# Performance work log

Measured on AMD Instinct MI355X. Metric: run time of the kernel, lower is better.

Reference implementation:

```python
import jax, jax.numpy as jnp
import numpy as np

B, S, I, H, O, L = 256, 512, 256, 256, 256, 64


def setup_inputs() -> dict:
    key = jax.random.key(0)
    ks = jax.random.split(key, 12)
    def lin(k, fan_in, fan_out):
        kw, kb = jax.random.split(k)
        lim = 1.0 / np.sqrt(fan_in)
        W = jax.random.uniform(kw, (fan_in, fan_out), jnp.float32, -lim, lim)
        b = jax.random.uniform(kb, (fan_out,), jnp.float32, -lim, lim)
        return W, b
    x = jax.random.normal(ks[0], (B, S, I), jnp.float32)
    W1x, b1x = lin(ks[1], I, H)   # rnn1.Wax
    W1a, b1a = lin(ks[2], H, H)   # rnn1.Waa
    W2x, b2x = lin(ks[3], O, H)   # rnn2.Wax
    W2a, b2a = lin(ks[4], H, H)   # rnn2.Waa
    Wy, by = lin(ks[5], H, O)     # Wya
    return {"x": x, "W1x": W1x, "b1x": b1x, "W1a": W1a, "b1a": b1a,
            "W2x": W2x, "b2x": b2x, "W2a": W2a, "b2a": b2a, "Wy": Wy, "by": by}


def reference(x, W1x, b1x, W1a, b1a, W2x, b2x, W2a, b2a, Wy, by):
    batch = x.shape[0]
    a0 = jnp.zeros((batch, W1a.shape[0]), x.dtype)  # a[:, -1] is zeros at encoder start

    # Encoder: a_t = tanh(Wax(x_t) + Waa(a_{t-1}))
    def enc_step(a, x_t):
        a = jnp.tanh(x_t @ W1x + b1x + a @ W1a + b1a)
        return a, None
    a_last, _ = jax.lax.scan(enc_step, a0, jnp.swapaxes(x, 0, 1))  # [S,B,I] scan

    # Torch code: y_pred[:,0] set from encoder, then decoder reads y_pred[:,i]
    # BEFORE overwriting it -> input is y0 at i=0, zeros for i>0.
    y0 = jax.nn.sigmoid(a_last @ Wy + by)  # [B,O]
    zero_in = jnp.zeros_like(y0)

    def dec_step(a, i):
        inp = jnp.where(i == 0, y0, zero_in)
        a = jnp.tanh(inp @ W2x + b2x + a @ W2a + b2a)
        y = jax.nn.sigmoid(a @ Wy + by)
        return a, y
    _, ys = jax.lax.scan(dec_step, a_last, jnp.arange(L))  # ys: [L,B,O]
    return jnp.swapaxes(ys, 0, 1)  # [B,L,O]
```

## Files before the change

kernel.cpp:

```cpp
#include <hip/hip_runtime.h>

typedef unsigned short u16;
typedef unsigned int   u32;
typedef __attribute__((ext_vector_type(8))) __bf16 bf16x8;
typedef __attribute__((ext_vector_type(8))) u16    u16x8;
typedef __attribute__((ext_vector_type(4))) float  f32x4;
typedef __attribute__((ext_vector_type(4))) u32    u32x4;
typedef __attribute__((ext_vector_type(2))) u32    u32x2;

#define MFMA16(a,b,c) __builtin_amdgcn_mfma_f32_16x16x32_bf16((a),(b),(c),0,0,0)
#define C_TANH 2.8853900817779268f
#define NL2E  -1.4426950408889634f

__device__ __forceinline__ float ubit(u32 x){ return __builtin_bit_cast(float, x); }
__device__ __forceinline__ u16 f2b(float f){
    u32 b = __builtin_bit_cast(u32, f);
    b += 0x7FFFu + ((b >> 16) & 1u);
    return (u16)(b >> 16);
}
__device__ __forceinline__ u32 pkbf(float a, float b){ return ((u32)f2b(b) << 16) | (u32)f2b(a); }
__device__ __forceinline__ u32 pk_away(float a, float b){
    u32 ua = (__builtin_bit_cast(u32, a) + 0x8000u) >> 16;
    u32 ub = (__builtin_bit_cast(u32, b) + 0x8000u) & 0xFFFF0000u;
    return ub | ua;
}
__device__ __forceinline__ void bar_lds(){ __asm__ volatile("s_waitcnt lgkmcnt(0)\n\ts_barrier" ::: "memory"); }

__global__ __launch_bounds__(256, 1) void k1_xw(const float* __restrict__ x, const float* __restrict__ w1x,
                                               const float* __restrict__ b1x, const float* __restrict__ b1a,
                                               u16* __restrict__ xpre)
{
    const int t = blockIdx.x;
    const int tid = threadIdx.x, lane = tid & 63, w = tid >> 6;
    const int l15 = lane & 15, q = lane >> 4;
    const int cw = w * 64;

    bf16x8 bw[4][8];
    f32x4 biasv[4];
    #pragma unroll
    for (int nt = 0; nt < 4; ++nt){
        const int n0 = cw + nt * 16 + q * 4;
        f32x4 bx = *(const f32x4*)(b1x + n0);
        f32x4 ba = *(const f32x4*)(b1a + n0);
        biasv[nt] = (bx + ba) * C_TANH;
        const int n = cw + nt * 16 + l15;
        #pragma unroll
        for (int ks = 0; ks < 8; ++ks){
            u16x8 tt;
            #pragma unroll
            for (int j = 0; j < 8; ++j) tt[j] = f2b(w1x[(ks * 32 + q * 8 + j) * 256 + n] * C_TANH);
            bw[nt][ks] = __builtin_bit_cast(bf16x8, tt);
        }
    }

    for (int blk = 0; blk < 16; ++blk){
        const int b0r = blk * 16;
        bf16x8 av[8];
        #pragma unroll
        for (int ks = 0; ks < 8; ++ks){
            const float* p = x + ((size_t)(b0r + l15) * 512 + t) * 256 + ks * 32 + q * 8;
            f32x4 v0 = *(const f32x4*)p;
            f32x4 v1 = *(const f32x4*)(p + 4);
            u32x4 dd = { pkbf(v0[0], v0[1]), pkbf(v0[2], v0[3]),
                         pkbf(v1[0], v1[1]), pkbf(v1[2], v1[3]) };
            av[ks] = __builtin_bit_cast(bf16x8, dd);
        }
        f32x4 acc[4];
        #pragma unroll
        for (int nt = 0; nt < 4; ++nt) acc[nt] = biasv[nt];
        #pragma unroll
        for (int ks = 0; ks < 8; ++ks)
            #pragma unroll
            for (int nt = 0; nt < 4; ++nt)
                acc[nt] = MFMA16(bw[nt][ks], av[ks], acc[nt]);
        const int bg = blk * 2 + (l15 >> 3);
        const size_t a16 = ((((size_t)t * 32 + bg) * 4 + w) * 32 + q * 8 + (l15 & 7)) * 16;
        u32x4 A  = { pkbf(acc[0][0], acc[0][1]), pkbf(acc[0][2], acc[0][3]),
                     pkbf(acc[1][0], acc[1][1]), pkbf(acc[1][2], acc[1][3]) };
        u32x4 Bv = { pkbf(acc[2][0], acc[2][1]), pkbf(acc[2][2], acc[2][3]),
                     pkbf(acc[3][0], acc[3][1]), pkbf(acc[3][2], acc[3][3]) };
        *(u32x4*)(xpre + a16)     = A;
        *(u32x4*)(xpre + a16 + 8) = Bv;
    }
}

__global__ __launch_bounds__(256, 1) void k2_enc(const float* __restrict__ w1a, const u16* __restrict__ xpre,
                                                u16* __restrict__ alast)
{
    __shared__ __align__(16) u16 st[2][8][264];
    const int tid = threadIdx.x, lane = tid & 63, w = tid >> 6;
    const int l15 = lane & 15, q = lane >> 4;
    const int lrow = l15 & 7, hi = l15 >> 3;
    const bool lo8 = (hi == 0);
    const int bg = blockIdx.x;

    bf16x8 bw[4][8];
    #pragma unroll
    for (int nt = 0; nt < 4; ++nt){
        const int n = w * 64 + nt * 16 + l15;
        #pragma unroll
        for (int ks = 0; ks < 8; ++ks){
            u16x8 tt;
            #pragma unroll
            for (int j = 0; j < 8; ++j) tt[j] = f2b(w1a[(ks * 32 + q * 8 + j) * 256 + n] * C_TANH);
            bw[nt][ks] = __builtin_bit_cast(bf16x8, tt);
        }
    }
    for (int i = tid; i < 8 * 264; i += 256) (&st[0][0][0])[i] = 0;
    __syncthreads();

    const u16* xp = xpre + ((((size_t)bg * 4 + w) * 32 + q * 8 + lrow) * 16);
    u32x4 c0 = *(const u32x4*)xp,           c1 = *(const u32x4*)(xp + 8);
    u32x4 a0 = *(const u32x4*)(xp + 65536), a1 = *(const u32x4*)(xp + 65536 + 8);

    const u16 (*sR)[264] = st[0];
    u16 (*sW)[264] = st[1];

    for (int t = 0; t < 512; ++t){
        const size_t tp = (size_t)((t + 2 < 512) ? t + 2 : 511) * 65536;
        u32x4 n0 = *(const u32x4*)(xp + tp);
        u32x4 n1 = *(const u32x4*)(xp + tp + 8);

        bf16x8 av[8];
        #pragma unroll
        for (int ks = 0; ks < 8; ++ks)
            av[ks] = *(const bf16x8*)&sR[lrow][ks * 32 + q * 8];

        f32x4 acc[4];
        #pragma unroll
        for (int nt = 0; nt < 4; ++nt){
            const u32x4 src = (nt < 2) ? c0 : c1;
            #pragma unroll
            for (int r = 0; r < 4; ++r){
                const u32 d = src[(nt & 1) * 2 + (r >> 1)];
                acc[nt][r] = ubit((r & 1) ? (d & 0xFFFF0000u) : (d << 16));
            }
        }
        #pragma unroll
        for (int ks = 0; ks < 8; ++ks)
            #pragma unroll
            for (int nt = 0; nt < 4; ++nt)
                acc[nt] = MFMA16(bw[nt][ks], av[ks], acc[nt]);

        #pragma unroll
        for (int p = 0; p < 2; ++p){
            float m[4];
            #pragma unroll
            for (int r = 0; r < 4; ++r){
                const float mv = lo8 ? acc[p][r] : acc[p + 2][r];
                const float e = __builtin_amdgcn_exp2f(mv);
                m[r] = 1.0f - 2.0f * __builtin_amdgcn_rcpf(e + 1.0f);
            }
            u32x2 hp = { pk_away(m[0], m[1]), pk_away(m[2], m[3]) };
            *(u32x2*)&sW[lrow][w * 64 + (p + 2 * hi) * 16 + q * 4] = hp;
        }

        c0 = a0; c1 = a1; a0 = n0; a1 = n1;
        bar_lds();
        const u16 (*tmp)[264] = sR; sR = (const u16(*)[264])sW; sW = (u16(*)[264])tmp;
    }
    {
        const int row = tid >> 5, c8 = (tid & 31) * 8;
        *(u32x4*)(alast + (size_t)(bg * 8 + row) * 256 + c8) = *(const u32x4*)&sR[row][c8];
    }
}

__global__ __launch_bounds__(256, 1) void k3_pre(const float* __restrict__ wy, const float* __restrict__ by,
                                                const float* __restrict__ w2x,
                                                const u16* __restrict__ alast, float* __restrict__ injws)
{
    __shared__ __align__(16) u16 st[16][264];
    __shared__ __align__(16) u16 y0s[16][264];
    const int tid = threadIdx.x, lane = tid & 63, w = tid >> 6;
    const int l15 = lane & 15, q = lane >> 4;
    const int lrow = l15 & 7, hi = l15 >> 3;
    const int bg = blockIdx.x;
    {
        const int row = tid >> 4, c = (tid & 15) * 16;
        #pragma unroll
        for (int j = 0; j < 2; ++j)
            *(u32x4*)&st[row][c + j * 8] = *(const u32x4*)(alast + (size_t)(bg * 16 + row) * 256 + c + j * 8);
    }
    __syncthreads();
    {
        bf16x8 bwy[4][8];
        f32x4 biasy[4];
        #pragma unroll
        for (int nt = 0; nt < 4; ++nt){
            const int n0 = w * 64 + nt * 16 + q * 4;
            biasy[nt] = (*(const f32x4*)(by + n0)) * NL2E;
            const int n = w * 64 + nt * 16 + l15;
            #pragma unroll
            for (int ks = 0; ks < 8; ++ks){
                u16x8 tt;
                #pragma unroll
                for (int j = 0; j < 8; ++j) tt[j] = f2b(wy[(ks * 32 + q * 8 + j) * 256 + n] * NL2E);
                bwy[nt][ks] = __builtin_bit_cast(bf16x8, tt);
            }
        }
        bf16x8 av[8];
        #pragma unroll
        for (int ks = 0; ks < 8; ++ks) av[ks] = *(const bf16x8*)&st[l15][ks * 32 + q * 8];
        f32x4 acc[4];
        #pragma unroll
        for (int nt = 0; nt < 4; ++nt) acc[nt] = biasy[nt];
        #pragma unroll
        for (int ks = 0; ks < 8; ++ks)
            #pragma unroll
            for (int nt = 0; nt < 4; ++nt) acc[nt] = MFMA16(bwy[nt][ks], av[ks], acc[nt]);
        #pragma unroll
        for (int nt = 0; nt < 4; ++nt){
            float y[4];
            #pragma unroll
            for (int r = 0; r < 4; ++r) y[r] = __builtin_amdgcn_rcpf(1.0f + __builtin_amdgcn_exp2f(acc[nt][r]));
            u32x2 hp = { pkbf(y[0], y[1]), pkbf(y[2], y[3]) };
            *(u32x2*)&y0s[l15][w * 64 + nt * 16 + q * 4] = hp;
        }
    }
    __syncthreads();
    {
        bf16x8 av[8];
        #pragma unroll
        for (int ks = 0; ks < 8; ++ks) av[ks] = *(const bf16x8*)&y0s[l15][ks * 32 + q * 8];
        f32x4 acc[4];
        #pragma unroll
        for (int nt = 0; nt < 4; ++nt) acc[nt] = (f32x4){0.f, 0.f, 0.f, 0.f};
        #pragma unroll
        for (int ks = 0; ks < 8; ++ks)
            #pragma unroll
            for (int nt = 0; nt < 4; ++nt){
                const int n = w * 64 + nt * 16 + l15;
                u16x8 tt;
                #pragma unroll
                for (int j = 0; j < 8; ++j) tt[j] = f2b(w2x[(ks * 32 + q * 8 + j) * 256 + n] * C_TANH);
                acc[nt] = MFMA16(__builtin_bit_cast(bf16x8, tt), av[ks], acc[nt]);
            }
        const size_t ib = ((((size_t)(bg * 2 + hi)) * 4 + w) * 32 + q * 8 + lrow) * 16;
        #pragma unroll
        for (int nt = 0; nt < 4; ++nt)
            *(f32x4*)(injws + ib + nt * 4) = acc[nt];
    }
}

__global__ __launch_bounds__(256, 1) void k3_rec(const float* __restrict__ w2a, const float* __restrict__ b2x,
                                                const float* __restrict__ b2a, const u16* __restrict__ alast,
                                                const float* __restrict__ injws, u16* __restrict__ astate)
{
    __shared__ __align__(16) u16 st[2][8][264];
    const int tid = threadIdx.x, lane = tid & 63, w = tid >> 6;
    const int l15 = lane & 15, q = lane >> 4;
    const int lrow = l15 & 7, hi = l15 >> 3;
    const bool lo8 = (hi == 0);
    const int bg = blockIdx.x;

    bf16x8 bw[4][8];
    f32x4 bias2[4];
    #pragma unroll
    for (int nt = 0; nt < 4; ++nt){
        const int n0 = w * 64 + nt * 16 + q * 4;
        f32x4 bx = *(const f32x4*)(b2x + n0);
        f32x4 ba = *(const f32x4*)(b2a + n0);
        bias2[nt] = (bx + ba) * C_TANH;
        const int n = w * 64 + nt * 16 + l15;
        #pragma unroll
        for (int ks = 0; ks < 8; ++ks){
            u16x8 tt;
            #pragma unroll
            for (int j = 0; j < 8; ++j) tt[j] = f2b(w2a[(ks * 32 + q * 8 + j) * 256 + n] * C_TANH);
            bw[nt][ks] = __builtin_bit_cast(bf16x8, tt);
        }
    }
    f32x4 ini[4];
    {
        const size_t ib = (((size_t)bg * 4 + w) * 32 + q * 8 + lrow) * 16;
        #pragma unroll
        for (int nt = 0; nt < 4; ++nt)
            ini[nt] = *(const f32x4*)(injws + ib + nt * 4) + bias2[nt];
    }
    {
        const int row = tid >> 5, c8 = (tid & 31) * 8;
        *(u32x4*)&st[0][row][c8] = *(const u32x4*)(alast + (size_t)(bg * 8 + row) * 256 + c8);
    }
    __syncthreads();

    const u16 (*sR)[264] = st[0];
    u16 (*sW)[264] = st[1];

    for (int i = 0; i < 64; ++i){
        bf16x8 av[8];
        #pragma unroll
        for (int ks = 0; ks < 8; ++ks) av[ks] = *(const bf16x8*)&sR[lrow][ks * 32 + q * 8];
        f32x4 acc[4];
        #pragma unroll
        for (int nt = 0; nt < 4; ++nt) acc[nt] = ini[nt];
        #pragma unroll
        for (int ks = 0; ks < 8; ++ks)
            #pragma unroll
            for (int nt = 0; nt < 4; ++nt) acc[nt] = MFMA16(bw[nt][ks], av[ks], acc[nt]);

        #pragma unroll
        for (int p = 0; p < 2; ++p){
            float m[4];
            #pragma unroll
            for (int r = 0; r < 4; ++r){
                const float mv = lo8 ? acc[p][r] : acc[p + 2][r];
                const float e = __builtin_amdgcn_exp2f(mv);
                m[r] = 1.0f - 2.0f * __builtin_amdgcn_rcpf(e + 1.0f);
            }
            u32x2 hp = { pk_away(m[0], m[1]), pk_away(m[2], m[3]) };
            *(u32x2*)&sW[lrow][w * 64 + (p + 2 * hi) * 16 + q * 4] = hp;
            *(u32x2*)(astate + ((size_t)i * 256 + bg * 8 + lrow) * 256
                              + w * 64 + (p + 2 * hi) * 16 + q * 4) = hp;
        }
        if (i == 0){
            #pragma unroll
            for (int nt = 0; nt < 4; ++nt) ini[nt] = bias2[nt];
        }
        bar_lds();
        const u16 (*tmp)[264] = sR; sR = (const u16(*)[264])sW; sW = (u16(*)[264])tmp;
    }
}

__global__ __launch_bounds__(256, 1) void k3_out(const float* __restrict__ wy, const float* __restrict__ by,
                                                const u16* __restrict__ astate, float* __restrict__ out)
{
    const int tid = threadIdx.x, lane = tid & 63, w = tid >> 6;
    const int l15 = lane & 15, q = lane >> 4;

    bf16x8 bwy[4][8];
    f32x4 biasy[4];
    #pragma unroll
    for (int nt = 0; nt < 4; ++nt){
        const int n0 = w * 64 + nt * 16 + q * 4;
        biasy[nt] = (*(const f32x4*)(by + n0)) * NL2E;
        const int n = w * 64 + nt * 16 + l15;
        #pragma unroll
        for (int ks = 0; ks < 8; ++ks){
            u16x8 tt;
            #pragma unroll
            for (int j = 0; j < 8; ++j) tt[j] = f2b(wy[(ks * 32 + q * 8 + j) * 256 + n] * NL2E);
            bwy[nt][ks] = __builtin_bit_cast(bf16x8, tt);
        }
    }
    #pragma unroll
    for (int tix = 0; tix < 4; ++tix){
        const int R0 = (blockIdx.x * 4 + tix) * 16;
        bf16x8 av[8];
        #pragma unroll
        for (int ks = 0; ks < 8; ++ks)
            av[ks] = *(const bf16x8*)(astate + (size_t)(R0 + l15) * 256 + ks * 32 + q * 8);
        f32x4 acc[4];
        #pragma unroll
        for (int nt = 0; nt < 4; ++nt) acc[nt] = biasy[nt];
        #pragma unroll
        for (int ks = 0; ks < 8; ++ks)
            #pragma unroll
            for (int nt = 0; nt < 4; ++nt) acc[nt] = MFMA16(bwy[nt][ks], av[ks], acc[nt]);
        const int R = R0 + l15, ii = R >> 8, b = R & 255;
        #pragma unroll
        for (int nt = 0; nt < 4; ++nt){
            f32x4 o4;
            #pragma unroll
            for (int r = 0; r < 4; ++r)
                o4[r] = __builtin_amdgcn_rcpf(1.0f + __builtin_amdgcn_exp2f(acc[nt][r]));
            *(f32x4*)(out + ((size_t)b * 64 + ii) * 256 + w * 64 + nt * 16 + q * 4) = o4;
        }
    }
}

extern "C" void kernel_launch(void* const* d_in, const int* in_sizes, int n_in,
                              void* d_out, int out_size, void* d_ws, size_t ws_size,
                              hipStream_t stream) {
    const float* x   = (const float*)d_in[0];
    const float* w1x = (const float*)d_in[1];
    const float* b1x = (const float*)d_in[2];
    const float* w1a = (const float*)d_in[3];
    const float* b1a = (const float*)d_in[4];
    const float* w2x = (const float*)d_in[5];
    const float* b2x = (const float*)d_in[6];
    const float* w2a = (const float*)d_in[7];
    const float* b2a = (const float*)d_in[8];
    const float* wy  = (const float*)d_in[9];
    const float* by  = (const float*)d_in[10];

    u16*   xpre   = (u16*)d_ws;
    u16*   astate = (u16*)d_ws;
    u16*   alast  = xpre + (size_t)512 * 16 * 512 * 8;
    float* injws  = (float*)(alast + 256 * 256);
    float* o      = (float*)d_out;

    k1_xw <<<512, 256, 0, stream>>>(x, w1x, b1x, b1a, xpre);
    k2_enc<<<32,  256, 0, stream>>>(w1a, xpre, alast);
    k3_pre<<<16,  256, 0, stream>>>(wy, by, w2x, alast, injws);
    k3_rec<<<32,  256, 0, stream>>>(w2a, b2x, b2a, alast, injws, astate);
    k3_out<<<256, 256, 0, stream>>>(wy, by, astate, o);
}
```

Before: 665.8 us.

## Split recurrent matmul across 8 waves per block in encoder and decoder

The serial encoder and decoder recurrences now run with 512 threads (8 waves) per block, each wave owning 32 output columns instead of 64. Each wave issues half as many MFMAs per timestep, which shortens the per-step critical path of the latency-bound recurrence. The xpre and injws layouts are changed to match the new per-wave column ownership. The cost is more waves taking part in each per-step barrier and each wave reloading the full hidden state from LDS.

```diff
diff --git a/kernel.cpp b/kernel.cpp
--- a/kernel.cpp
+++ b/kernel.cpp
@@ -33,6 +33,7 @@
     const int t = blockIdx.x;
     const int tid = threadIdx.x, lane = tid & 63, w = tid >> 6;
     const int l15 = lane & 15, q = lane >> 4;
+    const int lrow = l15 & 7, hi = l15 >> 3;
     const int cw = w * 64;
 
     bf16x8 bw[4][8];
@@ -73,31 +74,31 @@
             #pragma unroll
             for (int nt = 0; nt < 4; ++nt)
                 acc[nt] = MFMA16(bw[nt][ks], av[ks], acc[nt]);
-        const int bg = blk * 2 + (l15 >> 3);
-        const size_t a16 = ((((size_t)t * 32 + bg) * 4 + w) * 32 + q * 8 + (l15 & 7)) * 16;
-        u32x4 A  = { pkbf(acc[0][0], acc[0][1]), pkbf(acc[0][2], acc[0][3]),
-                     pkbf(acc[1][0], acc[1][1]), pkbf(acc[1][2], acc[1][3]) };
-        u32x4 Bv = { pkbf(acc[2][0], acc[2][1]), pkbf(acc[2][2], acc[2][3]),
-                     pkbf(acc[3][0], acc[3][1]), pkbf(acc[3][2], acc[3][3]) };
-        *(u32x4*)(xpre + a16)     = A;
-        *(u32x4*)(xpre + a16 + 8) = Bv;
-    }
-}
-
-__global__ __launch_bounds__(256, 1) void k2_enc(const float* __restrict__ w1a, const u16* __restrict__ xpre,
+        const int bg = blk * 2 + hi;
+        #pragma unroll
+        for (int p2 = 0; p2 < 2; ++p2){
+            const int w8 = w * 2 + p2;
+            const size_t a16 = ((((size_t)t * 32 + bg) * 8 + w8) * 32 + q * 8 + lrow) * 8;
+            u32x4 V = { pkbf(acc[p2 * 2][0], acc[p2 * 2][1]), pkbf(acc[p2 * 2][2], acc[p2 * 2][3]),
+                        pkbf(acc[p2 * 2 + 1][0], acc[p2 * 2 + 1][1]), pkbf(acc[p2 * 2 + 1][2], acc[p2 * 2 + 1][3]) };
+            *(u32x4*)(xpre + a16) = V;
+        }
+    }
+}
+
+__global__ __launch_bounds__(512, 2) void k2_enc(const float* __restrict__ w1a, const u16* __restrict__ xpre,
                                                 u16* __restrict__ alast)
 {
     __shared__ __align__(16) u16 st[2][8][264];
     const int tid = threadIdx.x, lane = tid & 63, w = tid >> 6;
     const int l15 = lane & 15, q = lane >> 4;
     const int lrow = l15 & 7, hi = l15 >> 3;
-    const bool lo8 = (hi == 0);
     const int bg = blockIdx.x;
 
-    bf16x8 bw[4][8];
-    #pragma unroll
-    for (int nt = 0; nt < 4; ++nt){
-        const int n = w * 64 + nt * 16 + l15;
+    bf16x8 bw[2][8];
+    #pragma unroll
+    for (int nt = 0; nt < 2; ++nt){
+        const int n = w * 32 + nt * 16 + l15;
         #pragma unroll
         for (int ks = 0; ks < 8; ++ks){
             u16x8 tt;
@@ -106,60 +107,54 @@
             bw[nt][ks] = __builtin_bit_cast(bf16x8, tt);
         }
     }
-    for (int i = tid; i < 8 * 264; i += 256) (&st[0][0][0])[i] = 0;
+    for (int i = tid; i < 8 * 264; i += 512) (&st[0][0][0])[i] = 0;
     __syncthreads();
 
-    const u16* xp = xpre + ((((size_t)bg * 4 + w) * 32 + q * 8 + lrow) * 16);
-    u32x4 c0 = *(const u32x4*)xp,           c1 = *(const u32x4*)(xp + 8);
-    u32x4 a0 = *(const u32x4*)(xp + 65536), a1 = *(const u32x4*)(xp + 65536 + 8);
+    const u16* xp = xpre + ((((size_t)bg) * 8 + w) * 32 + q * 8 + lrow) * 8;
+    u32x4 c = *(const u32x4*)xp;
+    u32x4 a = *(const u32x4*)(xp + 65536);
 
     const u16 (*sR)[264] = st[0];
     u16 (*sW)[264] = st[1];
 
     for (int t = 0; t < 512; ++t){
         const size_t tp = (size_t)((t + 2 < 512) ? t + 2 : 511) * 65536;
-        u32x4 n0 = *(const u32x4*)(xp + tp);
-        u32x4 n1 = *(const u32x4*)(xp + tp + 8);
+        u32x4 n_ = *(const u32x4*)(xp + tp);
 
         bf16x8 av[8];
         #pragma unroll
         for (int ks = 0; ks < 8; ++ks)
             av[ks] = *(const bf16x8*)&sR[lrow][ks * 32 + q * 8];
 
-        f32x4 acc[4];
-        #pragma unroll
-        for (int nt = 0; nt < 4; ++nt){
-            const u32x4 src = (nt < 2) ? c0 : c1;
+        f32x4 acc[2];
+        #pragma unroll
+        for (int nt = 0; nt < 2; ++nt)
             #pragma unroll
             for (int r = 0; r < 4; ++r){
-                const u32 d = src[(nt & 1) * 2 + (r >> 1)];
+                const u32 d = c[nt * 2 + (r >> 1)];
                 acc[nt][r] = ubit((r & 1) ? (d & 0xFFFF0000u) : (d << 16));
             }
-        }
-        #pragma unroll
-        for (int ks = 0; ks < 8; ++ks)
-            #pragma unroll
-            for (int nt = 0; nt < 4; ++nt)
+        #pragma unroll
+        for (int ks = 0; ks < 8; ++ks)
+            #pragma unroll
+            for (int nt = 0; nt < 2; ++nt)
                 acc[nt] = MFMA16(bw[nt][ks], av[ks], acc[nt]);
 
-        #pragma unroll
-        for (int p = 0; p < 2; ++p){
-            float m[4];
-            #pragma unroll
-            for (int r = 0; r < 4; ++r){
-                const float mv = lo8 ? acc[p][r] : acc[p + 2][r];
-                const float e = __builtin_amdgcn_exp2f(mv);
-                m[r] = 1.0f - 2.0f * __builtin_amdgcn_rcpf(e + 1.0f);
-            }
-            u32x2 hp = { pk_away(m[0], m[1]), pk_away(m[2], m[3]) };
-            *(u32x2*)&sW[lrow][w * 64 + (p + 2 * hi) * 16 + q * 4] = hp;
-        }
-
-        c0 = a0; c1 = a1; a0 = n0; a1 = n1;
+        float m[4];
+        #pragma unroll
+        for (int r = 0; r < 4; ++r){
+            const float mv = hi ? acc[1][r] : acc[0][r];
+            const float e = __builtin_amdgcn_exp2f(mv);
+            m[r] = 1.0f - 2.0f * __builtin_amdgcn_rcpf(e + 1.0f);
+        }
+        u32x2 hp = { pk_away(m[0], m[1]), pk_away(m[2], m[3]) };
+        *(u32x2*)&sW[lrow][w * 32 + hi * 16 + q * 4] = hp;
+
+        c = a; a = n_;
         bar_lds();
         const u16 (*tmp)[264] = sR; sR = (const u16(*)[264])sW; sW = (u16(*)[264])tmp;
     }
-    {
+    if (tid < 256){
         const int row = tid >> 5, c8 = (tid & 31) * 8;
         *(u32x4*)(alast + (size_t)(bg * 8 + row) * 256 + c8) = *(const u32x4*)&sR[row][c8];
     }
@@ -235,14 +230,16 @@
                 for (int j = 0; j < 8; ++j) tt[j] = f2b(w2x[(ks * 32 + q * 8 + j) * 256 + n] * C_TANH);
                 acc[nt] = MFMA16(__builtin_bit_cast(bf16x8, tt), av[ks], acc[nt]);
             }
-        const size_t ib = ((((size_t)(bg * 2 + hi)) * 4 + w) * 32 + q * 8 + lrow) * 16;
-        #pragma unroll
-        for (int nt = 0; nt < 4; ++nt)
-            *(f32x4*)(injws + ib + nt * 4) = acc[nt];
-    }
-}
-
-__global__ __launch_bounds__(256, 1) void k3_rec(const float* __restrict__ w2a, const float* __restrict__ b2x,
+        #pragma unroll
+        for (int nt = 0; nt < 4; ++nt){
+            const size_t ib = ((((size_t)(bg * 2 + hi)) * 8 + (size_t)(w * 2 + (nt >> 1))) * 32
+                               + q * 8 + lrow) * 8 + (nt & 1) * 4;
+            *(f32x4*)(injws + ib) = acc[nt];
+        }
+    }
+}
+
+__global__ __launch_bounds__(512, 2) void k3_rec(const float* __restrict__ w2a, const float* __restrict__ b2x,
                                                 const float* __restrict__ b2a, const u16* __restrict__ alast,
                                                 const float* __restrict__ injws, u16* __restrict__ astate)
 {
@@ -250,18 +247,17 @@
     const int tid = threadIdx.x, lane = tid & 63, w = tid >> 6;
     const int l15 = lane & 15, q = lane >> 4;
     const int lrow = l15 & 7, hi = l15 >> 3;
-    const bool lo8 = (hi == 0);
     const int bg = blockIdx.x;
 
-    bf16x8 bw[4][8];
-    f32x4 bias2[4];
-    #pragma unroll
-    for (int nt = 0; nt < 4; ++nt){
-        const int n0 = w * 64 + nt * 16 + q * 4;
+    bf16x8 bw[2][8];
+    f32x4 bias2[2];
+    #pragma unroll
+    for (int nt = 0; nt < 2; ++nt){
+        const int n0 = w * 32 + nt * 16 + q * 4;
         f32x4 bx = *(const f32x4*)(b2x + n0);
         f32x4 ba = *(const f32x4*)(b2a + n0);
         bias2[nt] = (bx + ba) * C_TANH;
-        const int n = w * 64 + nt * 16 + l15;
+        const int n = w * 32 + nt * 16 + l15;
         #pragma unroll
         for (int ks = 0; ks < 8; ++ks){
             u16x8 tt;
@@ -270,14 +266,14 @@
             bw[nt][ks] = __builtin_bit_cast(bf16x8, tt);
         }
     }
-    f32x4 ini[4];
+    f32x4 ini[2];
     {
-        const size_t ib = (((size_t)bg * 4 + w) * 32 + q * 8 + lrow) * 16;
-        #pragma unroll
-        for (int nt = 0; nt < 4; ++nt)
+        const size_t ib = (((size_t)bg * 8 + w) * 32 + q * 8 + lrow) * 8;
+        #pragma unroll
+        for (int nt = 0; nt < 2; ++nt)
             ini[nt] = *(const f32x4*)(injws + ib + nt * 4) + bias2[nt];
     }
-    {
+    if (tid < 256){
         const int row = tid >> 5, c8 = (tid & 31) * 8;
         *(u32x4*)&st[0][row][c8] = *(const u32x4*)(alast + (size_t)(bg * 8 + row) * 256 + c8);
     }
@@ -290,31 +286,29 @@
         bf16x8 av[8];
         #pragma unroll
         for (int ks = 0; ks < 8; ++ks) av[ks] = *(const bf16x8*)&sR[lrow][ks * 32 + q * 8];
-        f32x4 acc[4];
-        #pragma unroll
-        for (int nt = 0; nt < 4; ++nt) acc[nt] = ini[nt];
-        #pragma unroll
-        for (int ks = 0; ks < 8; ++ks)
-            #pragma unroll
-            for (int nt = 0; nt < 4; ++nt) acc[nt] = MFMA16(bw[nt][ks], av[ks], acc[nt]);
-
-        #pragma unroll
-        for (int p = 0; p < 2; ++p){
-            float m[4];
-            #pragma unroll
-            for (int r = 0; r < 4; ++r){
-                const float mv = lo8 ? acc[p][r] : acc[p + 2][r];
-                const float e = __builtin_amdgcn_exp2f(mv);
-                m[r] = 1.0f - 2.0f * __builtin_amdgcn_rcpf(e + 1.0f);
-            }
-            u32x2 hp = { pk_away(m[0], m[1]), pk_away(m[2], m[3]) };
-            *(u32x2*)&sW[lrow][w * 64 + (p + 2 * hi) * 16 + q * 4] = hp;
-            *(u32x2*)(astate + ((size_t)i * 256 + bg * 8 + lrow) * 256
-                              + w * 64 + (p + 2 * hi) * 16 + q * 4) = hp;
-        }
+        f32x4 acc[2];
+        #pragma unroll
+        for (int nt = 0; nt < 2; ++nt) acc[nt] = ini[nt];
+        #pragma unroll
+        for (int ks = 0; ks < 8; ++ks)
+            #pragma unroll
+            for (int nt = 0; nt < 2; ++nt) acc[nt] = MFMA16(bw[nt][ks], av[ks], acc[nt]);
+
+        float m[4];
+        #pragma unroll
+        for (int r = 0; r < 4; ++r){
+            const float mv = hi ? acc[1][r] : acc[0][r];
+            const float e = __builtin_amdgcn_exp2f(mv);
+            m[r] = 1.0f - 2.0f * __builtin_amdgcn_rcpf(e + 1.0f);
+        }
+        u32x2 hp = { pk_away(m[0], m[1]), pk_away(m[2], m[3]) };
+        *(u32x2*)&sW[lrow][w * 32 + hi * 16 + q * 4] = hp;
+        *(u32x2*)(astate + ((size_t)i * 256 + bg * 8 + lrow) * 256
+                          + w * 32 + hi * 16 + q * 4) = hp;
+
         if (i == 0){
             #pragma unroll
-            for (int nt = 0; nt < 4; ++nt) ini[nt] = bias2[nt];
+            for (int nt = 0; nt < 2; ++nt) ini[nt] = bias2[nt];
         }
         bar_lds();
         const u16 (*tmp)[264] = sR; sR = (const u16(*)[264])sW; sW = (u16(*)[264])tmp;
@@ -390,8 +384,8 @@
     float* o      = (float*)d_out;
 
     k1_xw <<<512, 256, 0, stream>>>(x, w1x, b1x, b1a, xpre);
-    k2_enc<<<32,  256, 0, stream>>>(w1a, xpre, alast);
+    k2_enc<<<32,  512, 0, stream>>>(w1a, xpre, alast);
     k3_pre<<<16,  256, 0, stream>>>(wy, by, w2x, alast, injws);
-    k3_rec<<<32,  256, 0, stream>>>(w2a, b2x, b2a, alast, injws, astate);
+    k3_rec<<<32,  512, 0, stream>>>(w2a, b2x, b2a, alast, injws, astate);
     k3_out<<<256, 256, 0, stream>>>(wy, by, astate, o);
 }
```

After: 585.4 us. 1.14x faster.
